# Optimization experiments

Measured on AMD Instinct MI355X. Metric: run time of the kernel, lower is better.

The kernel has to match this reference:

```python
import jax, jax.numpy as jnp
import numpy as np

D_MODEL = 1024
N_REG = 8
D_REG = 32
LN_EPS = 1e-5


def setup_inputs() -> dict:
    key = jax.random.key(0)
    ks = jax.random.split(key, 14)
    s = 0.02
    return {
        "x": jax.random.normal(ks[0], (8, 2048, D_MODEL), dtype=jnp.float32),
        "ln_w": jnp.ones((D_MODEL,), jnp.float32),
        "ln_b": jnp.zeros((D_MODEL,), jnp.float32),
        "Wrq": jax.random.normal(ks[1], (N_REG, D_MODEL), jnp.float32) * s,
        "brq": jax.random.normal(ks[2], (N_REG,), jnp.float32) * s,
        "Wrp": jax.random.normal(ks[3], (D_MODEL, D_REG), jnp.float32) * s,
        "brp": jax.random.normal(ks[4], (D_MODEL,), jnp.float32) * s,
        "Wwq": jax.random.normal(ks[5], (N_REG, D_MODEL), jnp.float32) * s,
        "bwq": jax.random.normal(ks[6], (N_REG,), jnp.float32) * s,
        "Wwv": jax.random.normal(ks[7], (D_REG, D_MODEL), jnp.float32) * s,
        "bwv": jax.random.normal(ks[8], (D_REG,), jnp.float32) * s,
        "Wwg": jax.random.normal(ks[9], (1, D_MODEL), jnp.float32) * s,
        "bwg": jnp.full((1,), -3.0, jnp.float32),
        "mix": jnp.asarray(0.001, jnp.float32),
    }


def _layernorm(x, w, b):
    mu = jnp.mean(x, axis=-1, keepdims=True)
    var = jnp.mean(jnp.square(x - mu), axis=-1, keepdims=True)
    return (x - mu) * jax.lax.rsqrt(var + LN_EPS) * w + b


def _forward(x, ln_w, ln_b, Wrq, brq, Wrp, brp, Wwq, bwq, Wwv, bwv, Wwg, bwg, mix):
    B, L, D = x.shape
    h = _layernorm(x, ln_w, ln_b)  # (B,L,D)
    # Precompute all per-timestep projections as big GEMMs (same math as per-step Linear)
    r_w = jax.nn.softmax(jnp.einsum("bld,rd->blr", h, Wrq) + brq, axis=-1)  # (B,L,R)
    w_w = jax.nn.softmax(jnp.einsum("bld,rd->blr", h, Wwq) + bwq, axis=-1)  # (B,L,R)
    w_v = jnp.einsum("bld,kd->blk", h, Wwv) + bwv                           # (B,L,Dr)
    w_g = jax.nn.sigmoid(jnp.einsum("bld,od->blo", h, Wwg) + bwg)           # (B,L,1)

    def step(registers, inputs):
        rw_t, ww_t, wv_t, wg_t = inputs  # (B,R), (B,R), (B,Dr), (B,1)
        r_v = jnp.einsum("br,brd->bd", rw_t, registers)  # read (B,Dr)
        us = (ww_t * wg_t)[..., None]                     # (B,R,1)
        new_regs = (1.0 - us) * registers + us * wv_t[:, None, :]
        return new_regs, r_v

    init_regs = jnp.zeros((B, N_REG, D_REG), x.dtype)
    seq = (
        jnp.moveaxis(r_w, 1, 0),
        jnp.moveaxis(w_w, 1, 0),
        jnp.moveaxis(w_v, 1, 0),
        jnp.moveaxis(w_g, 1, 0),
    )
    _, r_vs = jax.lax.scan(step, init_regs, seq)  # (L,B,Dr)
    r_vs = jnp.moveaxis(r_vs, 0, 1)               # (B,L,Dr)
    r_out = jnp.einsum("blk,dk->bld", r_vs, Wrp) + brp  # read_proj
    return mix * r_out


def reference(x, ln_w, ln_b, Wrq, brq, Wrp, brp, Wwq, bwq, Wwv, bwv, Wwg, bwg, mix):
    return _forward(x, ln_w, ln_b, Wrq, brq, Wrp, brp, Wwq, bwq, Wwv, bwv, Wwg, bwg, mix)
```

## Files before the change

### kernel.cpp

```cpp
#include <hip/hip_runtime.h>

#define D_MODEL 1024
#define L_SEQ   2048
#define N_BATCH 8
#define N_TOK   (N_BATCH * L_SEQ)
#define N_REGS  8
#define D_REG   32
#define LN_EPS  1e-5f

#define KC      32
#define XSTR    65
#define XQ      (KC * XSTR)
#define SSTR    57

#define HSTEP   16
#define N_HALF  128

__device__ __forceinline__ float wred(float v) {
    #pragma unroll
    for (int off = 32; off > 0; off >>= 1) v += __shfl_xor(v, off, 64);
    return v;
}

__device__ __forceinline__ float sigmoidf(float z) {
    return 1.f / (1.f + expf(-z));
}

__global__ __launch_bounds__(256) void k_prep(
    const float* __restrict__ ln_w, const float* __restrict__ ln_b,
    const float* __restrict__ Wrq,  const float* __restrict__ brq,
    const float* __restrict__ Wwq,  const float* __restrict__ bwq,
    const float* __restrict__ Wwv,  const float* __restrict__ bwv,
    const float* __restrict__ Wwg,  const float* __restrict__ bwg,
    float* __restrict__ Wpp, float* __restrict__ c1, float* __restrict__ c2)
{
    const int f = blockIdx.x;
    const int g = f / 13, i = f % 13;

    const float* wrow = nullptr; float bias = 0.f;
    if (f < 8)        { wrow = Wrq + f * D_MODEL;        bias = brq[f]; }
    else if (f < 16)  { wrow = Wwq + (f - 8) * D_MODEL;  bias = bwq[f - 8]; }
    else if (f == 16) { wrow = Wwg;                      bias = bwg[0]; }
    else if (f < 49)  { wrow = Wwv + (f - 17) * D_MODEL; bias = bwv[f - 17]; }

    float p1 = 0.f, p2 = 0.f;
    #pragma unroll
    for (int j = 0; j < 4; ++j) {
        const int k = j * 256 + threadIdx.x;
        float w  = wrow ? wrow[k] : 0.f;
        float wg = w * ln_w[k];
        Wpp[((size_t)(g * D_MODEL + k)) * 16 + i] = wg;
        p1 += wg;
        p2 = fmaf(w, ln_b[k], p2);
    }
    p1 = wred(p1); p2 = wred(p2);

    __shared__ float r1[4], r2[4];
    const int l = threadIdx.x & 63, w = threadIdx.x >> 6;
    if (l == 0) { r1[w] = p1; r2[w] = p2; }
    __syncthreads();
    if (threadIdx.x == 0) {
        c1[f] = r1[0] + r1[1] + r1[2] + r1[3];
        c2[f] = r2[0] + r2[1] + r2[2] + r2[3] + bias;
    }
}

template<int STATS>
__device__ __forceinline__ void proj_chunk(
    const float* __restrict__ lx,
    const float4* __restrict__ wr0,
    int lane, float acc[13], float& st)
{
    #pragma unroll 4
    for (int k = 0; k < KC; ++k) {
        const float xs = lx[k * XSTR + lane];
        const float4* wr = wr0 + (k << 2);
        float4 wa = wr[0], wb = wr[1], wc = wr[2];
        float  wd = reinterpret_cast<const float*>(wr)[12];
        acc[0]  = fmaf(xs, wa.x, acc[0]);
        acc[1]  = fmaf(xs, wa.y, acc[1]);
        acc[2]  = fmaf(xs, wa.z, acc[2]);
        acc[3]  = fmaf(xs, wa.w, acc[3]);
        acc[4]  = fmaf(xs, wb.x, acc[4]);
        acc[5]  = fmaf(xs, wb.y, acc[5]);
        acc[6]  = fmaf(xs, wb.z, acc[6]);
        acc[7]  = fmaf(xs, wb.w, acc[7]);
        acc[8]  = fmaf(xs, wc.x, acc[8]);
        acc[9]  = fmaf(xs, wc.y, acc[9]);
        acc[10] = fmaf(xs, wc.z, acc[10]);
        acc[11] = fmaf(xs, wc.w, acc[11]);
        acc[12] = fmaf(xs, wd,   acc[12]);
        if (STATS == 1) st += xs;
        if (STATS == 2) st = fmaf(xs, xs, st);
    }
}

__global__ __launch_bounds__(1024) void k_lnproj3(
    const float* __restrict__ x,
    const float* __restrict__ Wpp,
    const float* __restrict__ c1, const float* __restrict__ c2,
    float* __restrict__ rw_o, float* __restrict__ us_o, float* __restrict__ wv_o)
{
    extern __shared__ float lds[];
    float* Sb = lds + 2 * 4 * XQ;

    const int tid  = threadIdx.x;
    const int lane = tid & 63;
    const int wv   = tid >> 6;
    const int g    = wv & 3;
    const int kh   = wv >> 2;
    const int tok0 = blockIdx.x * 64;

    const int gs  = __builtin_amdgcn_readfirstlane(g);
    const int khs = __builtin_amdgcn_readfirstlane(kh);

    const int tq  = tid & 255;
    const int row = tq >> 3;
    const int c4  = tq & 7;

    const float4* x4 = reinterpret_cast<const float4*>(x);

    float4 xg[2];
    float acc[13];
    #pragma unroll
    for (int i = 0; i < 13; ++i) acc[i] = 0.f;
    float st = 0.f;

    const size_t gbase = (size_t)(tok0 + row) * 256 + khs * 64 + c4;

    {
        xg[0] = x4[gbase];
        xg[1] = x4[gbase + 32 * 256];
        float* dst = lds + khs * XQ + (c4 * 4) * XSTR;
        #pragma unroll
        for (int p = 0; p < 2; ++p) {
            const int r = row + 32 * p;
            dst[0 * XSTR + r] = xg[p].x;
            dst[1 * XSTR + r] = xg[p].y;
            dst[2 * XSTR + r] = xg[p].z;
            dst[3 * XSTR + r] = xg[p].w;
        }
    }
    __syncthreads();

    for (int c = 0; c < 8; ++c) {
        if (c < 7)  {
            xg[0] = x4[gbase + (size_t)(c + 1) * 8];
            xg[1] = x4[gbase + (size_t)(c + 1) * 8 + 32 * 256];
        }

        const float*  lx  = lds + ((c & 1) * 4 + khs) * XQ;
        const float4* wr0 = reinterpret_cast<const float4*>(Wpp)
                          + ((gs * D_MODEL + khs * 256 + c * KC) << 2);
        if (gs == 1)      proj_chunk<1>(lx, wr0, lane, acc, st);
        else if (gs == 2) proj_chunk<2>(lx, wr0, lane, acc, st);
        else              proj_chunk<0>(lx, wr0, lane, acc, st);

        if (c < 7) {
            float* dst = lds + (((c + 1) & 1) * 4 + khs) * XQ + (c4 * 4) * XSTR;
            #pragma unroll
            for (int p = 0; p < 2; ++p) {
                const int r = row + 32 * p;
                dst[0 * XSTR + r] = xg[p].x;
                dst[1 * XSTR + r] = xg[p].y;
                dst[2 * XSTR + r] = xg[p].z;
                dst[3 * XSTR + r] = xg[p].w;
            }
        }
        __syncthreads();
    }

    if (kh == 0) {
        #pragma unroll
        for (int i = 0; i < 13; ++i) Sb[lane * SSTR + g * 13 + i] = acc[i];
        if (g == 1) Sb[lane * SSTR + 52] = st;
        if (g == 2) Sb[lane * SSTR + 53] = st;
    }
    __syncthreads();
    #pragma unroll
    for (int ph = 1; ph < 4; ++ph) {
        if (kh == ph) {
            #pragma unroll
            for (int i = 0; i < 13; ++i) Sb[lane * SSTR + g * 13 + i] += acc[i];
            if (g == 1) Sb[lane * SSTR + 52] += st;
            if (g == 2) Sb[lane * SSTR + 53] += st;
        }
        __syncthreads();
    }

    if (tid < 256) {
        const int t  = tid & 63;
        const int q  = tid >> 6;
        const int tg = blockIdx.x * 64 + t;
        const float* St = Sb + t * SSTR;

        const float tsum = St[52], tss = St[53];
        const float mu  = tsum * (1.f / D_MODEL);
        const float var = tss * (1.f / D_MODEL) - mu * mu;
        const float rs  = rsqrtf(var + LN_EPS);

        if (q == 0) {
            float lg[8];
            #pragma unroll
            for (int r = 0; r < 8; ++r)
                lg[r] = rs * (St[r] - mu * c1[r]) + c2[r];
            float m = lg[0];
            #pragma unroll
            for (int r = 1; r < 8; ++r) m = fmaxf(m, lg[r]);
            float sm = 0.f;
            #pragma unroll
            for (int r = 0; r < 8; ++r) { lg[r] = expf(lg[r] - m); sm += lg[r]; }
            float inv = 1.f / sm;
            float4* o = reinterpret_cast<float4*>(rw_o + (size_t)tg * 8);
            o[0] = make_float4(lg[0]*inv, lg[1]*inv, lg[2]*inv, lg[3]*inv);
            o[1] = make_float4(lg[4]*inv, lg[5]*inv, lg[6]*inv, lg[7]*inv);
        } else if (q == 1) {
            float lg[8];
            #pragma unroll
            for (int r = 0; r < 8; ++r)
                lg[r] = rs * (St[8 + r] - mu * c1[8 + r]) + c2[8 + r];
            float gl = rs * (St[16] - mu * c1[16]) + c2[16];
            float m = lg[0];
            #pragma unroll
            for (int r = 1; r < 8; ++r) m = fmaxf(m, lg[r]);
            float sm = 0.f;
            #pragma unroll
            for (int r = 0; r < 8; ++r) { lg[r] = expf(lg[r] - m); sm += lg[r]; }
            float inv = sigmoidf(gl) / sm;
            float4* o = reinterpret_cast<float4*>(us_o + (size_t)tg * 8);
            o[0] = make_float4(lg[0]*inv, lg[1]*inv, lg[2]*inv, lg[3]*inv);
            o[1] = make_float4(lg[4]*inv, lg[5]*inv, lg[6]*inv, lg[7]*inv);
        } else {
            const int f0 = 17 + (q - 2) * 16;
            float4* o = reinterpret_cast<float4*>(wv_o + (size_t)tg * 32 + (q - 2) * 16);
            #pragma unroll
            for (int jq = 0; jq < 4; ++jq) {
                float v0 = rs * (St[f0 + jq*4 + 0] - mu * c1[f0 + jq*4 + 0]) + c2[f0 + jq*4 + 0];
                float v1 = rs * (St[f0 + jq*4 + 1] - mu * c1[f0 + jq*4 + 1]) + c2[f0 + jq*4 + 1];
                float v2 = rs * (St[f0 + jq*4 + 2] - mu * c1[f0 + jq*4 + 2]) + c2[f0 + jq*4 + 2];
                float v3 = rs * (St[f0 + jq*4 + 3] - mu * c1[f0 + jq*4 + 3]) + c2[f0 + jq*4 + 3];
                o[jq] = make_float4(v0, v1, v2, v3);
            }
        }
    }
}

__global__ __launch_bounds__(1024) void k_scan(
    const float* __restrict__ us, const float* __restrict__ wv,
    float* __restrict__ S0)
{
    __shared__ float S_us[L_SEQ];
    __shared__ float lA[N_HALF];
    __shared__ float lB[N_HALF * 32];

    const int tid = threadIdx.x;
    const int b   = blockIdx.x >> 3;
    const int r   = blockIdx.x & 7;

    #pragma unroll
    for (int i = 0; i < 2; ++i) {
        const int t = i * 1024 + tid;
        S_us[t] = us[((size_t)(b * L_SEQ + t)) * 8 + r];
    }
    __syncthreads();

    const int k  = tid & 31;
    const int hb = (tid >> 5) * 4;
    #pragma unroll
    for (int j = 0; j < 4; ++j) {
        const int h  = hb + j;
        const int t0 = h * HSTEP;
        const float* wvp = wv + ((size_t)(b * L_SEQ + t0)) * 32 + k;

        float Aacc = 1.f, Bacc = 0.f;
        #pragma unroll
        for (int gq = 0; gq < 2; ++gq) {
            float wl[8], ul[8];
            #pragma unroll
            for (int e = 0; e < 8; ++e) {
                wl[e] = wvp[(gq * 8 + e) * 32];
                ul[e] = S_us[t0 + gq * 8 + e];
            }
            #pragma unroll
            for (int e = 0; e < 8; ++e) {
                float a = 1.f - ul[e];
                Aacc *= a;
                Bacc = fmaf(a, Bacc, ul[e] * wl[e]);
            }
        }
        lB[h * 32 + k] = Bacc;
        if (k == 0) lA[h] = Aacc;
    }
    __syncthreads();

    if (tid < 32) {
        float stv = 0.f;
        float* S0p = S0 + ((size_t)(b * 8 + r) * N_HALF) * 32 + tid;
        for (int h = 0; h < N_HALF; ++h) {
            S0p[h * 32] = stv;
            stv = fmaf(lA[h], stv, lB[h * 32 + tid]);
        }
    }
}

__global__ __launch_bounds__(256) void k_replay2(
    const float* __restrict__ rw, const float* __restrict__ us,
    const float* __restrict__ wv, const float* __restrict__ S0,
    float* __restrict__ rvs)
{
    const int gid = blockIdx.x * 256 + threadIdx.x;
    const int k   = gid & 31;
    const int hu  = gid >> 5;
    const int b   = hu >> 7;
    const int ch2 = hu & 127;

    float s[8];
    #pragma unroll
    for (int r = 0; r < 8; ++r)
        s[r] = S0[((size_t)((b * 8 + r) * N_HALF) + ch2) * 32 + k];

    const int t0 = b * L_SEQ + ch2 * HSTEP;
    const float* rwp = rw + (size_t)t0 * 8;
    const float* usp = us + (size_t)t0 * 8;
    const float* wvp = wv + (size_t)t0 * 32 + k;
    float*       rvp = rvs + (size_t)t0 * 32 + k;

    #pragma unroll
    for (int g4 = 0; g4 < 4; ++g4) {
        float4 r0[4], r1[4], u0[4], u1[4];
        float  wl[4];
        #pragma unroll
        for (int j = 0; j < 4; ++j) {
            const int t = g4 * 4 + j;
            r0[j] = reinterpret_cast<const float4*>(rwp + t * 8)[0];
            r1[j] = reinterpret_cast<const float4*>(rwp + t * 8)[1];
            u0[j] = reinterpret_cast<const float4*>(usp + t * 8)[0];
            u1[j] = reinterpret_cast<const float4*>(usp + t * 8)[1];
            wl[j] = wvp[t * 32];
        }
        #pragma unroll
        for (int j = 0; j < 4; ++j) {
            const int t = g4 * 4 + j;
            float rv = r0[j].x*s[0] + r0[j].y*s[1] + r0[j].z*s[2] + r0[j].w*s[3]
                     + r1[j].x*s[4] + r1[j].y*s[5] + r1[j].z*s[6] + r1[j].w*s[7];
            rvp[t * 32] = rv;
            const float w = wl[j];
            s[0] = fmaf(u0[j].x, w - s[0], s[0]);
            s[1] = fmaf(u0[j].y, w - s[1], s[1]);
            s[2] = fmaf(u0[j].z, w - s[2], s[2]);
            s[3] = fmaf(u0[j].w, w - s[3], s[3]);
            s[4] = fmaf(u1[j].x, w - s[4], s[4]);
            s[5] = fmaf(u1[j].y, w - s[5], s[5]);
            s[6] = fmaf(u1[j].z, w - s[6], s[6]);
            s[7] = fmaf(u1[j].w, w - s[7], s[7]);
        }
    }
}

__global__ __launch_bounds__(256) void k_outproj2(
    const float* __restrict__ rvs, const float* __restrict__ Wrp,
    const float* __restrict__ brp, const float* __restrict__ mix_p,
    float* __restrict__ out)
{
    const int d0   = threadIdx.x * 4;
    const int tok0 = blockIdx.x * 64;

    float4 wr[4][8];
    #pragma unroll
    for (int i = 0; i < 4; ++i)
        #pragma unroll
        for (int q = 0; q < 8; ++q)
            wr[i][q] = reinterpret_cast<const float4*>(Wrp)[(size_t)(d0 + i) * 8 + q];

    const float4 bias = *reinterpret_cast<const float4*>(brp + d0);
    const float  mix  = mix_p[0];

    for (int t = 0; t < 64; ++t) {
        const float4* rv = reinterpret_cast<const float4*>(rvs + (size_t)(tok0 + t) * 32);
        float4 v[8];
        #pragma unroll
        for (int q = 0; q < 8; ++q) v[q] = rv[q];

        float acc[4] = {0.f, 0.f, 0.f, 0.f};
        #pragma unroll
        for (int i = 0; i < 4; ++i)
            #pragma unroll
            for (int q = 0; q < 8; ++q)
                acc[i] += wr[i][q].x*v[q].x + wr[i][q].y*v[q].y
                        + wr[i][q].z*v[q].z + wr[i][q].w*v[q].w;

        float4 o = make_float4(mix * (acc[0] + bias.x), mix * (acc[1] + bias.y),
                               mix * (acc[2] + bias.z), mix * (acc[3] + bias.w));
        *reinterpret_cast<float4*>(out + (size_t)(tok0 + t) * D_MODEL + d0) = o;
    }
}

extern "C" void kernel_launch(void* const* d_in, const int* in_sizes, int n_in,
                              void* d_out, int out_size, void* d_ws, size_t ws_size,
                              hipStream_t stream)
{
    const float* x    = (const float*)d_in[0];
    const float* ln_w = (const float*)d_in[1];
    const float* ln_b = (const float*)d_in[2];
    const float* Wrq  = (const float*)d_in[3];
    const float* brq  = (const float*)d_in[4];
    const float* Wrp  = (const float*)d_in[5];
    const float* brp  = (const float*)d_in[6];
    const float* Wwq  = (const float*)d_in[7];
    const float* bwq  = (const float*)d_in[8];
    const float* Wwv  = (const float*)d_in[9];
    const float* bwv  = (const float*)d_in[10];
    const float* Wwg  = (const float*)d_in[11];
    const float* bwg  = (const float*)d_in[12];
    const float* mix  = (const float*)d_in[13];
    float* out = (float*)d_out;

    float* ws   = (float*)d_ws;
    float* rw_b = ws;
    float* us_b = ws + 131072;
    float* wv_b = ws + 262144;
    float* S0_b = ws + 786432;
    float* rv_b = ws + 1048576;
    float* Wpp  = rv_b;
    float* c1_b = rv_b + 65536;
    float* c2_b = rv_b + 65600;

    const size_t lds_bytes = (size_t)(2 * 4 * XQ + 64 * SSTR) * 4;

    k_prep<<<52, 256, 0, stream>>>(ln_w, ln_b, Wrq, brq, Wwq, bwq,
                                   Wwv, bwv, Wwg, bwg, Wpp, c1_b, c2_b);
    k_lnproj3<<<256, 1024, lds_bytes, stream>>>(x, Wpp, c1_b, c2_b,
                                                rw_b, us_b, wv_b);
    k_scan   <<<64, 1024, 0, stream>>>(us_b, wv_b, S0_b);
    k_replay2<<<128, 256, 0, stream>>>(rw_b, us_b, wv_b, S0_b, rv_b);
    k_outproj2<<<256, 256, 0, stream>>>(rv_b, Wrp, brp, mix, out);
}
```

Measured before the change: 105.2 us.

## Retile output projection: more blocks, fewer tokens each, stage read vectors in LDS

The output projection kernel moves from 256 blocks of 256 threads (4 output columns, 64 tokens each) to 1024 blocks of 512 threads (2 columns, 16 tokens each). Each block stages its 16 read vectors in shared memory, so threads no longer each load them redundantly from global memory. This is meant to raise occupancy and parallelism on a kernel bound by the 64 MB output write, and to cut per-thread register pressure. In exchange, each Wrp row is reloaded by four times as many blocks and the stores become float2 instead of float4.

```diff
diff --git a/kernel.cpp b/kernel.cpp
--- a/kernel.cpp
+++ b/kernel.cpp
@@ -357,41 +357,42 @@
     }
 }
 
-__global__ __launch_bounds__(256) void k_outproj2(
+__global__ __launch_bounds__(512) void k_outproj3(
     const float* __restrict__ rvs, const float* __restrict__ Wrp,
     const float* __restrict__ brp, const float* __restrict__ mix_p,
     float* __restrict__ out)
 {
-    const int d0   = threadIdx.x * 4;
-    const int tok0 = blockIdx.x * 64;
-
-    float4 wr[4][8];
-    #pragma unroll
-    for (int i = 0; i < 4; ++i)
-        #pragma unroll
-        for (int q = 0; q < 8; ++q)
-            wr[i][q] = reinterpret_cast<const float4*>(Wrp)[(size_t)(d0 + i) * 8 + q];
-
-    const float4 bias = *reinterpret_cast<const float4*>(brp + d0);
+    __shared__ float lrv[16 * 32];
+
+    const int tid  = threadIdx.x;
+    const int d0   = tid * 2;
+    const int tok0 = blockIdx.x * 16;
+
+    lrv[tid] = rvs[(size_t)tok0 * 32 + tid];
+
+    float4 w0[8], w1[8];
+    #pragma unroll
+    for (int q = 0; q < 8; ++q) {
+        w0[q] = reinterpret_cast<const float4*>(Wrp)[(size_t)d0 * 8 + q];
+        w1[q] = reinterpret_cast<const float4*>(Wrp)[(size_t)(d0 + 1) * 8 + q];
+    }
+    const float2 bias = *reinterpret_cast<const float2*>(brp + d0);
     const float  mix  = mix_p[0];
 
-    for (int t = 0; t < 64; ++t) {
-        const float4* rv = reinterpret_cast<const float4*>(rvs + (size_t)(tok0 + t) * 32);
-        float4 v[8];
-        #pragma unroll
-        for (int q = 0; q < 8; ++q) v[q] = rv[q];
-
-        float acc[4] = {0.f, 0.f, 0.f, 0.f};
-        #pragma unroll
-        for (int i = 0; i < 4; ++i)
-            #pragma unroll
-            for (int q = 0; q < 8; ++q)
-                acc[i] += wr[i][q].x*v[q].x + wr[i][q].y*v[q].y
-                        + wr[i][q].z*v[q].z + wr[i][q].w*v[q].w;
-
-        float4 o = make_float4(mix * (acc[0] + bias.x), mix * (acc[1] + bias.y),
-                               mix * (acc[2] + bias.z), mix * (acc[3] + bias.w));
-        *reinterpret_cast<float4*>(out + (size_t)(tok0 + t) * D_MODEL + d0) = o;
+    __syncthreads();
+
+    #pragma unroll 4
+    for (int t = 0; t < 16; ++t) {
+        const float4* v4 = reinterpret_cast<const float4*>(lrv + t * 32);
+        float a0 = 0.f, a1 = 0.f;
+        #pragma unroll
+        for (int q = 0; q < 8; ++q) {
+            float4 v = v4[q];
+            a0 += w0[q].x*v.x + w0[q].y*v.y + w0[q].z*v.z + w0[q].w*v.w;
+            a1 += w1[q].x*v.x + w1[q].y*v.y + w1[q].z*v.z + w1[q].w*v.w;
+        }
+        float2 o = make_float2(mix * (a0 + bias.x), mix * (a1 + bias.y));
+        *reinterpret_cast<float2*>(out + (size_t)(tok0 + t) * D_MODEL + d0) = o;
     }
 }
 
@@ -433,5 +434,5 @@
                                                 rw_b, us_b, wv_b);
     k_scan   <<<64, 1024, 0, stream>>>(us_b, wv_b, S0_b);
     k_replay2<<<128, 256, 0, stream>>>(rw_b, us_b, wv_b, S0_b, rv_b);
-    k_outproj2<<<256, 256, 0, stream>>>(rv_b, Wrp, brp, mix, out);
-}
+    k_outproj3<<<1024, 512, 0, stream>>>(rv_b, Wrp, brp, mix, out);
+}
```

Result: faster. 103.1 us (-2.0%).
